# Performance work log

Measured on AMD Instinct MI355X. Metric: run time of the kernel, lower is better.

## Reference

```python
import jax, jax.numpy as jnp
import numpy as np

B = 65536
IN2 = 256      # input_shape * 2
H2 = 512       # rnn_hidden_dim * 2
A = 32         # n_actions


def setup_inputs() -> dict:
    key = jax.random.key(0)
    ks = jax.random.split(key, 12)
    s = lambda k, shape, fan: jax.random.normal(k, shape, jnp.float32) / np.sqrt(fan)
    return {
        "inputs": jax.random.normal(ks[0], (B, IN2), jnp.float32),
        "hidden_state": jax.random.normal(ks[1], (B, H2), jnp.float32),
        "W1": s(ks[2], (H2, IN2), IN2),
        "b1": jnp.zeros((H2,), jnp.float32),
        "W_ih": s(ks[3], (3 * H2, H2), H2),
        "W_hh": s(ks[4], (3 * H2, H2), H2),
        "b_ih": jnp.zeros((3 * H2,), jnp.float32),
        "b_hh": jnp.zeros((3 * H2,), jnp.float32),
        "W21": s(ks[5], (A, H2), H2),
        "b21": jnp.zeros((A,), jnp.float32),
        "W22": s(ks[6], (A, H2), H2),
        "b22": jnp.zeros((A,), jnp.float32),
    }


def _forward(inputs, hidden_state, W1, b1, W_ih, W_hh, b_ih, b_hh, W21, b21, W22, b22):
    # fc1 + ReLU
    x = jax.nn.relu(inputs @ W1.T + b1)                      # [B, H2]
    h_in = hidden_state.reshape(-1, H2)
    # PyTorch GRUCell semantics
    gi = x @ W_ih.T + b_ih                                   # [B, 3*H2]
    gh = h_in @ W_hh.T + b_hh                                # [B, 3*H2]
    i_r, i_z, i_n = jnp.split(gi, 3, axis=1)
    h_r, h_z, h_n = jnp.split(gh, 3, axis=1)
    r = jax.nn.sigmoid(i_r + h_r)
    z = jax.nn.sigmoid(i_z + h_z)
    n = jnp.tanh(i_n + r * h_n)
    h = (1.0 - z) * n + z * h_in                             # [B, H2]
    # two Q heads
    q1 = h @ W21.T + b21                                     # [B, A]
    q2 = h @ W22.T + b22                                     # [B, A]
    # vectorized row-interleave (replaces the nested Python loop)
    q = jnp.stack([q1, q2], axis=1).reshape(2 * q1.shape[0], q1.shape[1])  # [2B, A]
    return q, h


def reference(inputs, hidden_state, W1, b1, W_ih, W_hh, b_ih, b_hh, W21, b21, W22, b22):
    return _forward(inputs, hidden_state, W1, b1, W_ih, W_hh, b_ih, b_hh, W21, b21, W22, b22)
```

## Files before the change

kernel.cpp:

```cpp
#include <hip/hip_runtime.h>


#define BATCH 65536
#define IN2   256
#define H2    512
#define NA    32
#define QELEMS (2 * BATCH * NA)

typedef float  f32x4  __attribute__((ext_vector_type(4)));
typedef short  short8 __attribute__((ext_vector_type(8)));
typedef __bf16 bf16x8 __attribute__((ext_vector_type(8)));

__device__ __forceinline__ f32x4 mfma16(short8 a, short8 b, f32x4 c) {
  return __builtin_amdgcn_mfma_f32_16x16x32_bf16(
      __builtin_bit_cast(bf16x8, a), __builtin_bit_cast(bf16x8, b), c, 0, 0, 0);
}

__device__ __forceinline__ unsigned short f2bf(float f) {
  union { float f; unsigned u; } v; v.f = f;
  unsigned r = v.u + 0x7fffu + ((v.u >> 16) & 1u);
  return (unsigned short)(r >> 16);
}
__device__ __forceinline__ float bf2f(unsigned short u) {
  union { unsigned u; float f; } v; v.u = ((unsigned)u) << 16; return v.f;
}

__device__ __forceinline__ void gload16(const void* g, void* l) {
  __builtin_amdgcn_global_load_lds(
      (const __attribute__((address_space(1))) void*)g,
      (__attribute__((address_space(3))) void*)l, 16, 0, 0);
}

__device__ __forceinline__ float sigm(float x) {
  return 1.f / (1.f + __expf(-x));
}
__device__ __forceinline__ float tanh_fast(float x) {
  float t = __expf(-2.f * fabsf(x));
  float r = (1.f - t) / (1.f + t);
  return x >= 0.f ? r : -r;
}

__global__ void cvt_kernel(const float* __restrict__ s,
                           unsigned short* __restrict__ d, int n4) {
  for (int i = blockIdx.x * blockDim.x + threadIdx.x; i < n4;
       i += gridDim.x * blockDim.x) {
    float4 f = ((const float4*)s)[i];
    ushort4 o;
    o.x = f2bf(f.x); o.y = f2bf(f.y); o.z = f2bf(f.z); o.w = f2bf(f.w);
    ((ushort4*)d)[i] = o;
  }
}

__global__ void cvtw_kernel(const float* __restrict__ W1,
                            const float* __restrict__ Wih,
                            const float* __restrict__ Whh,
                            const float* __restrict__ W21,
                            const float* __restrict__ W22,
                            unsigned short* __restrict__ dW1,
                            unsigned short* __restrict__ dWih,
                            unsigned short* __restrict__ dWhh,
                            unsigned short* __restrict__ dW21,
                            unsigned short* __restrict__ dW22) {
  int i = blockIdx.x * blockDim.x + threadIdx.x;
  const float* s; unsigned short* d; int local;
  if      (i < 32768)  { s = W1;  d = dW1;  local = i; }
  else if (i < 229376) { s = Wih; d = dWih; local = i - 32768; }
  else if (i < 425984) { s = Whh; d = dWhh; local = i - 229376; }
  else if (i < 430080) { s = W21; d = dW21; local = i - 425984; }
  else if (i < 434176) { s = W22; d = dW22; local = i - 430080; }
  else return;
  float4 f = ((const float4*)s)[local];
  ushort4 o;
  o.x = f2bf(f.x); o.y = f2bf(f.y); o.z = f2bf(f.z); o.w = f2bf(f.w);
  ((ushort4*)d)[local] = o;
}

__global__ __launch_bounds__(256, 2)
void fc1_kernel(const float* __restrict__ A,
                const unsigned short* __restrict__ W,
                const float* __restrict__ bias,
                unsigned short* __restrict__ X) {
  __shared__ unsigned short As[128][72];
  __shared__ unsigned short Bs[64][72];
  const int tid  = threadIdx.x;
  const int lane = tid & 63, wid = tid >> 6;
  const int l16 = lane & 15, kg = (lane >> 4) * 8, rbase = (lane >> 4) * 4;
  const int row0 = blockIdx.x * 128;
  const int col0 = blockIdx.y * 64;
  const int wrow = (wid >> 1) * 64;
  const int wcol = (wid & 1) * 32;

  f32x4 acc[4][2] = {};

  for (int k0 = 0; k0 < IN2; k0 += 64) {
#pragma unroll
    for (int c = 0; c < 4; ++c) {
      int idx = tid + c * 256;
      int r = idx >> 3, k8 = idx & 7;
      const float* src = &A[(size_t)(row0 + r) * IN2 + k0 + k8 * 8];
      float4 f0 = *(const float4*)src;
      float4 f1 = *(const float4*)(src + 4);
      uint4 o;
      o.x = f2bf(f0.x) | ((unsigned)f2bf(f0.y) << 16);
      o.y = f2bf(f0.z) | ((unsigned)f2bf(f0.w) << 16);
      o.z = f2bf(f1.x) | ((unsigned)f2bf(f1.y) << 16);
      o.w = f2bf(f1.z) | ((unsigned)f2bf(f1.w) << 16);
      *(uint4*)&As[r][k8 * 8] = o;
    }
#pragma unroll
    for (int c = 0; c < 2; ++c) {
      int idx = tid + c * 256;
      int r = idx >> 3, k8 = idx & 7;
      *(uint4*)&Bs[r][k8 * 8] =
          *(const uint4*)&W[(size_t)(col0 + r) * IN2 + k0 + k8 * 8];
    }
    __syncthreads();
#pragma unroll
    for (int kk = 0; kk < 64; kk += 32) {
      short8 af[4], bf[2];
#pragma unroll
      for (int m = 0; m < 4; ++m)
        af[m] = *(const short8*)&As[wrow + m * 16 + l16][kk + kg];
#pragma unroll
      for (int n = 0; n < 2; ++n)
        bf[n] = *(const short8*)&Bs[wcol + n * 16 + l16][kk + kg];
#pragma unroll
      for (int m = 0; m < 4; ++m)
#pragma unroll
        for (int n = 0; n < 2; ++n)
          acc[m][n] = mfma16(af[m], bf[n], acc[m][n]);
    }
    __syncthreads();
  }

#pragma unroll
  for (int m = 0; m < 4; ++m)
#pragma unroll
    for (int n = 0; n < 2; ++n) {
      int col = col0 + wcol + n * 16 + l16;
      float bv = bias[col];
#pragma unroll
      for (int e = 0; e < 4; ++e) {
        int row = row0 + wrow + m * 16 + rbase + e;
        float v = acc[m][n][e] + bv;
        v = v > 0.f ? v : 0.f;
        X[(size_t)row * H2 + col] = f2bf(v);
      }
    }
}

__global__ __launch_bounds__(256, 2)
void gru_kernel(const unsigned short* __restrict__ X16,
                const unsigned short* __restrict__ H16,
                const unsigned short* __restrict__ Wih,
                const unsigned short* __restrict__ Whh,
                const float* __restrict__ b_ih,
                const float* __restrict__ b_hh,
                float* __restrict__ out_h,
                unsigned short* __restrict__ h16b) {
  __shared__ unsigned short lds[40960];
  char* ldsb = (char*)lds;

  const int tid  = threadIdx.x;
  const int lane = tid & 63, wid = tid >> 6;
  const int l16 = lane & 15;
  const int row0 = blockIdx.x * 128;
  const int j0   = blockIdx.y * 64;
  const int wrow = (wid >> 1) * 64;
  const int wcol = (wid & 1) * 32;

  const int lr   = lane >> 3;
  const int scol = ((lane & 7) ^ (lr & 7)) * 8;
  const unsigned short* gx = X16 + (size_t)(row0 + wid * 32 + lr) * H2 + scol;
  const unsigned short* gh = H16 + (size_t)(row0 + wid * 32 + lr) * H2 + scol;

  f32x4 accR[4][2] = {}, accZ[4][2] = {}, accIN[4][2] = {}, accHN[4][2] = {};

  for (int k0 = 0; k0 < H2; k0 += 64) {
#pragma unroll
    for (int i = 0; i < 4; ++i) {
      gload16(gx + k0 + i * 8 * H2, ldsb + (wid * 4 + i) * 1024);
      gload16(gh + k0 + i * 8 * H2, ldsb + 16384 + (wid * 4 + i) * 1024);
    }
#pragma unroll
    for (int i = 0; i < 12; ++i) {
      int g = wid * 12 + i;
      int s = g >> 3;
      int r = (g & 7) * 8 + lr;
      const unsigned short* src =
          (s < 3) ? Wih + (size_t)(s * H2 + j0 + r) * H2
                  : Whh + (size_t)((s - 3) * H2 + j0 + r) * H2;
      gload16(src + k0 + scol, ldsb + 32768 + g * 1024);
    }
    __syncthreads();

#pragma unroll
    for (int kk = 0; kk < 64; kk += 32) {
      const int cch = (kk >> 3) + (lane >> 4);
      short8 ax[4], ah[4];
#pragma unroll
      for (int m = 0; m < 4; ++m) {
        int r = wrow + m * 16 + l16;
        int off = r * 128 + ((cch ^ (r & 7)) << 4);
        ax[m] = *(const short8*)(ldsb + off);
        ah[m] = *(const short8*)(ldsb + 16384 + off);
      }
#pragma unroll
      for (int n = 0; n < 2; ++n) {
        int rr = wcol + n * 16 + l16;
        int woff = 32768 + rr * 128 + ((cch ^ (rr & 7)) << 4);
        short8 b0 = *(const short8*)(ldsb + woff);
        short8 b3 = *(const short8*)(ldsb + woff + 3 * 8192);
#pragma unroll
        for (int m = 0; m < 4; ++m) {
          accR[m][n] = mfma16(ax[m], b0, accR[m][n]);
          accR[m][n] = mfma16(ah[m], b3, accR[m][n]);
        }
        short8 b1 = *(const short8*)(ldsb + woff + 1 * 8192);
        short8 b4 = *(const short8*)(ldsb + woff + 4 * 8192);
#pragma unroll
        for (int m = 0; m < 4; ++m) {
          accZ[m][n] = mfma16(ax[m], b1, accZ[m][n]);
          accZ[m][n] = mfma16(ah[m], b4, accZ[m][n]);
        }
        short8 b2 = *(const short8*)(ldsb + woff + 2 * 8192);
        short8 b5 = *(const short8*)(ldsb + woff + 5 * 8192);
#pragma unroll
        for (int m = 0; m < 4; ++m) {
          accIN[m][n] = mfma16(ax[m], b2, accIN[m][n]);
          accHN[m][n] = mfma16(ah[m], b5, accHN[m][n]);
        }
      }
    }
    __syncthreads();
  }

  const int rbase = (lane >> 4) * 4;
#pragma unroll
  for (int n = 0; n < 2; ++n) {
    int j = j0 + wcol + n * 16 + l16;
    float brr = b_ih[j] + b_hh[j];
    float bzz = b_ih[H2 + j] + b_hh[H2 + j];
    float bin = b_ih[2 * H2 + j];
    float bhn = b_hh[2 * H2 + j];
#pragma unroll
    for (int m = 0; m < 4; ++m) {
#pragma unroll
      for (int e = 0; e < 4; ++e) {
        int row = row0 + wrow + m * 16 + rbase + e;
        float r  = sigm(accR[m][n][e] + brr);
        float z  = sigm(accZ[m][n][e] + bzz);
        float nn = tanh_fast(accIN[m][n][e] + bin + r * (accHN[m][n][e] + bhn));
        float hp = bf2f(H16[(size_t)row * H2 + j]);
        float h  = (1.f - z) * nn + z * hp;
        out_h[(size_t)row * H2 + j] = h;
        if (h16b) h16b[(size_t)row * H2 + j] = f2bf(h);
      }
    }
  }
}

__global__ __launch_bounds__(256, 2)
void heads_bf16_kernel(const unsigned short* __restrict__ Hsrc,
                       const unsigned short* __restrict__ Wq1,
                       const unsigned short* __restrict__ Wq2,
                       const float* __restrict__ b21,
                       const float* __restrict__ b22,
                       float* __restrict__ outq) {
  __shared__ unsigned short Hs[64][72];
  __shared__ unsigned short Wq[2][32][72];
  const int tid  = threadIdx.x;
  const int lane = tid & 63, wid = tid >> 6;
  const int l16 = lane & 15, kg = (lane >> 4) * 8, rbase = (lane >> 4) * 4;
  const int row0 = blockIdx.x * 64;
  const int wrow = wid * 16;

  f32x4 acc[2][2] = {};

  for (int k0 = 0; k0 < H2; k0 += 64) {
#pragma unroll
    for (int c = 0; c < 2; ++c) {
      int idx = tid + c * 256;
      int r = idx >> 3, k8 = idx & 7;
      *(uint4*)&Hs[r][k8 * 8] =
          *(const uint4*)&Hsrc[(size_t)(row0 + r) * H2 + k0 + k8 * 8];
    }
#pragma unroll
    for (int c = 0; c < 2; ++c) {
      int idx = tid + c * 256;
      int slab = idx >> 8, rem = idx & 255;
      int r = rem >> 3, k8 = rem & 7;
      const unsigned short* src = slab ? Wq2 : Wq1;
      *(uint4*)&Wq[slab][r][k8 * 8] =
          *(const uint4*)&src[(size_t)r * H2 + k0 + k8 * 8];
    }
    __syncthreads();
#pragma unroll
    for (int kk = 0; kk < 64; kk += 32) {
      short8 a = *(const short8*)&Hs[wrow + l16][kk + kg];
#pragma unroll
      for (int hd = 0; hd < 2; ++hd)
#pragma unroll
        for (int n = 0; n < 2; ++n) {
          short8 b = *(const short8*)&Wq[hd][n * 16 + l16][kk + kg];
          acc[hd][n] = mfma16(a, b, acc[hd][n]);
        }
    }
    __syncthreads();
  }

#pragma unroll
  for (int hd = 0; hd < 2; ++hd)
#pragma unroll
    for (int n = 0; n < 2; ++n) {
      int col = n * 16 + l16;
      float bv = hd ? b22[col] : b21[col];
#pragma unroll
      for (int e = 0; e < 4; ++e) {
        int row = row0 + wrow + rbase + e;
        outq[(size_t)(2 * row + hd) * NA + col] = acc[hd][n][e] + bv;
      }
    }
}

__global__ __launch_bounds__(256, 2)
void heads_f32_kernel(const float* __restrict__ Hsrc,
                      const unsigned short* __restrict__ Wq1,
                      const unsigned short* __restrict__ Wq2,
                      const float* __restrict__ b21,
                      const float* __restrict__ b22,
                      float* __restrict__ outq) {
  __shared__ unsigned short Hs[64][72];
  __shared__ unsigned short Wq[2][32][72];
  const int tid  = threadIdx.x;
  const int lane = tid & 63, wid = tid >> 6;
  const int l16 = lane & 15, kg = (lane >> 4) * 8, rbase = (lane >> 4) * 4;
  const int row0 = blockIdx.x * 64;
  const int wrow = wid * 16;

  f32x4 acc[2][2] = {};

  for (int k0 = 0; k0 < H2; k0 += 64) {
#pragma unroll
    for (int c = 0; c < 4; ++c) {
      int idx = tid + c * 256;
      int r = idx >> 4, c4 = idx & 15;
      float4 f = *(const float4*)&Hsrc[(size_t)(row0 + r) * H2 + k0 + c4 * 4];
      ushort4 o;
      o.x = f2bf(f.x); o.y = f2bf(f.y); o.z = f2bf(f.z); o.w = f2bf(f.w);
      *(ushort4*)&Hs[r][c4 * 4] = o;
    }
#pragma unroll
    for (int c = 0; c < 2; ++c) {
      int idx = tid + c * 256;
      int slab = idx >> 8, rem = idx & 255;
      int r = rem >> 3, k8 = rem & 7;
      const unsigned short* src = slab ? Wq2 : Wq1;
      *(uint4*)&Wq[slab][r][k8 * 8] =
          *(const uint4*)&src[(size_t)r * H2 + k0 + k8 * 8];
    }
    __syncthreads();
#pragma unroll
    for (int kk = 0; kk < 64; kk += 32) {
      short8 a = *(const short8*)&Hs[wrow + l16][kk + kg];
#pragma unroll
      for (int hd = 0; hd < 2; ++hd)
#pragma unroll
        for (int n = 0; n < 2; ++n) {
          short8 b = *(const short8*)&Wq[hd][n * 16 + l16][kk + kg];
          acc[hd][n] = mfma16(a, b, acc[hd][n]);
        }
    }
    __syncthreads();
  }

#pragma unroll
  for (int hd = 0; hd < 2; ++hd)
#pragma unroll
    for (int n = 0; n < 2; ++n) {
      int col = n * 16 + l16;
      float bv = hd ? b22[col] : b21[col];
#pragma unroll
      for (int e = 0; e < 4; ++e) {
        int row = row0 + wrow + rbase + e;
        outq[(size_t)(2 * row + hd) * NA + col] = acc[hd][n][e] + bv;
      }
    }
}

extern "C" void kernel_launch(void* const* d_in, const int* in_sizes, int n_in,
                              void* d_out, int out_size, void* d_ws,
                              size_t ws_size, hipStream_t stream) {
  (void)in_sizes; (void)n_in; (void)out_size;
  const float* inputs = (const float*)d_in[0];
  const float* hidden = (const float*)d_in[1];
  const float* W1     = (const float*)d_in[2];
  const float* b1     = (const float*)d_in[3];
  const float* W_ih   = (const float*)d_in[4];
  const float* W_hh   = (const float*)d_in[5];
  const float* b_ih   = (const float*)d_in[6];
  const float* b_hh   = (const float*)d_in[7];
  const float* W21    = (const float*)d_in[8];
  const float* b21    = (const float*)d_in[9];
  const float* W22    = (const float*)d_in[10];
  const float* b22    = (const float*)d_in[11];
  float* out = (float*)d_out;

  char* ws = (char*)d_ws;
  size_t off = 0;
  unsigned short* h16   = (unsigned short*)(ws + off); off += (size_t)BATCH * H2 * 2;
  unsigned short* x16   = (unsigned short*)(ws + off); off += (size_t)BATCH * H2 * 2;
  unsigned short* W1_16 = (unsigned short*)(ws + off); off += (size_t)H2 * IN2 * 2;
  unsigned short* Wih16 = (unsigned short*)(ws + off); off += (size_t)3 * H2 * H2 * 2;
  unsigned short* Whh16 = (unsigned short*)(ws + off); off += (size_t)3 * H2 * H2 * 2;
  unsigned short* W2116 = (unsigned short*)(ws + off); off += (size_t)NA * H2 * 2;
  unsigned short* W2216 = (unsigned short*)(ws + off); off += (size_t)NA * H2 * 2;
  size_t base_need = off;
  unsigned short* h16b = nullptr;
  if (ws_size >= base_need + (size_t)BATCH * H2 * 2)
    h16b = (unsigned short*)(ws + base_need);

  cvt_kernel<<<8192, 256, 0, stream>>>(hidden, h16, BATCH * H2 / 4);
  cvtw_kernel<<<1696, 256, 0, stream>>>(W1, W_ih, W_hh, W21, W22,
                                        W1_16, Wih16, Whh16, W2116, W2216);

  fc1_kernel<<<dim3(BATCH / 128, H2 / 64), 256, 0, stream>>>(inputs, W1_16, b1, x16);

  float* out_h = out + QELEMS;
  gru_kernel<<<dim3(BATCH / 128, H2 / 64), 256, 0, stream>>>(
      x16, h16, Wih16, Whh16, b_ih, b_hh, out_h, h16b);

  if (h16b)
    heads_bf16_kernel<<<BATCH / 64, 256, 0, stream>>>(h16b, W2116, W2216, b21, b22, out);
  else
    heads_f32_kernel<<<BATCH / 64, 256, 0, stream>>>(out_h, W2116, W2216, b21, b22, out);
}
```

Baseline: 644.2 us.

## Double-buffer fc1/GRU GEMMs, merge conversion kernels, restructure heads kernel

Merges the hidden-state and weight bf16 conversion kernels into one launch. Rewrites fc1 and the GRU GEMM with K=32 double-buffered LDS stages, an XOR swizzle, s_setprio around the MFMAs, and a block-index remap that groups column tiles for L2 reuse. The heads kernels now keep both Q-head weight matrices resident in LDS and read H fragments straight from global memory, with 128 rows per block. The aim is to overlap global loads with MFMA work and cut launch and sync overhead, at the cost of more LDS per block (80 KB for GRU) and possible occupancy limits.

```diff
diff --git a/kernel.cpp b/kernel.cpp
--- a/kernel.cpp
+++ b/kernel.cpp
@@ -10,6 +10,7 @@
 typedef float  f32x4  __attribute__((ext_vector_type(4)));
 typedef short  short8 __attribute__((ext_vector_type(8)));
 typedef __bf16 bf16x8 __attribute__((ext_vector_type(8)));
+typedef unsigned short ushort_t;
 
 __device__ __forceinline__ f32x4 mfma16(short8 a, short8 b, f32x4 c) {
   return __builtin_amdgcn_mfma_f32_16x16x32_bf16(
@@ -40,99 +41,117 @@
   return x >= 0.f ? r : -r;
 }
 
-__global__ void cvt_kernel(const float* __restrict__ s,
-                           unsigned short* __restrict__ d, int n4) {
-  for (int i = blockIdx.x * blockDim.x + threadIdx.x; i < n4;
+__global__ void cvt_all(const float* __restrict__ hid,
+                        const float* __restrict__ W1,
+                        const float* __restrict__ Wih,
+                        const float* __restrict__ Whh,
+                        const float* __restrict__ W21,
+                        const float* __restrict__ W22,
+                        ushort_t* __restrict__ h16,
+                        ushort_t* __restrict__ dW1,
+                        ushort_t* __restrict__ dWih,
+                        ushort_t* __restrict__ dWhh,
+                        ushort_t* __restrict__ dW21,
+                        ushort_t* __restrict__ dW22) {
+  for (int i = blockIdx.x * blockDim.x + threadIdx.x; i < 8822784;
        i += gridDim.x * blockDim.x) {
-    float4 f = ((const float4*)s)[i];
+    const float* s; ushort_t* d; int lo;
+    if (i < 8388608) { s = hid; d = h16; lo = i; }
+    else {
+      int k = i - 8388608;
+      if      (k < 32768)  { s = W1;  d = dW1;  lo = k; }
+      else if (k < 229376) { s = Wih; d = dWih; lo = k - 32768; }
+      else if (k < 425984) { s = Whh; d = dWhh; lo = k - 229376; }
+      else if (k < 430080) { s = W21; d = dW21; lo = k - 425984; }
+      else                 { s = W22; d = dW22; lo = k - 430080; }
+    }
+    float4 f = ((const float4*)s)[lo];
     ushort4 o;
     o.x = f2bf(f.x); o.y = f2bf(f.y); o.z = f2bf(f.z); o.w = f2bf(f.w);
-    ((ushort4*)d)[i] = o;
-  }
-}
-
-__global__ void cvtw_kernel(const float* __restrict__ W1,
-                            const float* __restrict__ Wih,
-                            const float* __restrict__ Whh,
-                            const float* __restrict__ W21,
-                            const float* __restrict__ W22,
-                            unsigned short* __restrict__ dW1,
-                            unsigned short* __restrict__ dWih,
-                            unsigned short* __restrict__ dWhh,
-                            unsigned short* __restrict__ dW21,
-                            unsigned short* __restrict__ dW22) {
-  int i = blockIdx.x * blockDim.x + threadIdx.x;
-  const float* s; unsigned short* d; int local;
-  if      (i < 32768)  { s = W1;  d = dW1;  local = i; }
-  else if (i < 229376) { s = Wih; d = dWih; local = i - 32768; }
-  else if (i < 425984) { s = Whh; d = dWhh; local = i - 229376; }
-  else if (i < 430080) { s = W21; d = dW21; local = i - 425984; }
-  else if (i < 434176) { s = W22; d = dW22; local = i - 430080; }
-  else return;
-  float4 f = ((const float4*)s)[local];
-  ushort4 o;
-  o.x = f2bf(f.x); o.y = f2bf(f.y); o.z = f2bf(f.z); o.w = f2bf(f.w);
-  ((ushort4*)d)[local] = o;
-}
-
-__global__ __launch_bounds__(256, 2)
+    ((ushort4*)d)[lo] = o;
+  }
+}
+
+__global__ __launch_bounds__(256, 4)
 void fc1_kernel(const float* __restrict__ A,
-                const unsigned short* __restrict__ W,
+                const ushort_t* __restrict__ W,
                 const float* __restrict__ bias,
-                unsigned short* __restrict__ X) {
-  __shared__ unsigned short As[128][72];
-  __shared__ unsigned short Bs[64][72];
+                ushort_t* __restrict__ X) {
+  __shared__ char ldsb[24576];
   const int tid  = threadIdx.x;
   const int lane = tid & 63, wid = tid >> 6;
-  const int l16 = lane & 15, kg = (lane >> 4) * 8, rbase = (lane >> 4) * 4;
-  const int row0 = blockIdx.x * 128;
-  const int col0 = blockIdx.y * 64;
+  const int l16  = lane & 15;
+  const int bid  = blockIdx.x;
+  const int lin  = (bid & 7) * 512 + (bid >> 3);
+  const int row0 = (lin >> 3) * 128;
+  const int col0 = (lin & 7) * 64;
   const int wrow = (wid >> 1) * 64;
   const int wcol = (wid & 1) * 32;
+  const int lr   = lane >> 2;
+  const int sc8  = ((lane & 3) ^ (lr & 3)) * 8;
+  const int rdx  = (((lane >> 4) ^ (lane & 3)) << 4);
 
   f32x4 acc[4][2] = {};
-
-  for (int k0 = 0; k0 < IN2; k0 += 64) {
-#pragma unroll
-    for (int c = 0; c < 4; ++c) {
-      int idx = tid + c * 256;
-      int r = idx >> 3, k8 = idx & 7;
-      const float* src = &A[(size_t)(row0 + r) * IN2 + k0 + k8 * 8];
-      float4 f0 = *(const float4*)src;
-      float4 f1 = *(const float4*)(src + 4);
+  float4 ra[2], rb[2];
+  char* buf0 = ldsb;
+  char* buf1 = ldsb + 12288;
+
+  auto LOADA = [&](int t) {
+#pragma unroll
+    for (int i = 0; i < 2; ++i) {
+      const float* p =
+          A + (size_t)(row0 + (wid * 2 + i) * 16 + lr) * IN2 + t * 32 + sc8;
+      ra[i] = *(const float4*)p;
+      rb[i] = *(const float4*)(p + 4);
+    }
+  };
+  auto GW = [&](int t, char* buf) {
+    const int jrow = col0 + wid * 16 + lr;
+    gload16(W + (size_t)jrow * IN2 + t * 32 + sc8, buf + 8192 + wid * 1024);
+  };
+  auto WRITEA = [&](char* buf) {
+#pragma unroll
+    for (int i = 0; i < 2; ++i) {
       uint4 o;
-      o.x = f2bf(f0.x) | ((unsigned)f2bf(f0.y) << 16);
-      o.y = f2bf(f0.z) | ((unsigned)f2bf(f0.w) << 16);
-      o.z = f2bf(f1.x) | ((unsigned)f2bf(f1.y) << 16);
-      o.w = f2bf(f1.z) | ((unsigned)f2bf(f1.w) << 16);
-      *(uint4*)&As[r][k8 * 8] = o;
-    }
-#pragma unroll
-    for (int c = 0; c < 2; ++c) {
-      int idx = tid + c * 256;
-      int r = idx >> 3, k8 = idx & 7;
-      *(uint4*)&Bs[r][k8 * 8] =
-          *(const uint4*)&W[(size_t)(col0 + r) * IN2 + k0 + k8 * 8];
-    }
+      o.x = f2bf(ra[i].x) | ((unsigned)f2bf(ra[i].y) << 16);
+      o.y = f2bf(ra[i].z) | ((unsigned)f2bf(ra[i].w) << 16);
+      o.z = f2bf(rb[i].x) | ((unsigned)f2bf(rb[i].y) << 16);
+      o.w = f2bf(rb[i].z) | ((unsigned)f2bf(rb[i].w) << 16);
+      *(uint4*)(buf + (wid * 2 + i) * 1024 + lane * 16) = o;
+    }
+  };
+  auto COMPUTE = [&](const char* buf) {
+    short8 af[4], bf[2];
+#pragma unroll
+    for (int m = 0; m < 4; ++m)
+      af[m] = *(const short8*)(buf + (wrow + m * 16 + l16) * 64 + rdx);
+#pragma unroll
+    for (int n = 0; n < 2; ++n)
+      bf[n] = *(const short8*)(buf + 8192 + (wcol + n * 16 + l16) * 64 + rdx);
+    __builtin_amdgcn_s_setprio(1);
+#pragma unroll
+    for (int m = 0; m < 4; ++m)
+#pragma unroll
+      for (int n = 0; n < 2; ++n)
+        acc[m][n] = mfma16(af[m], bf[n], acc[m][n]);
+    __builtin_amdgcn_s_setprio(0);
+  };
+
+  LOADA(0); GW(0, buf0); WRITEA(buf0);
+  __syncthreads();
+#pragma unroll 1
+  for (int t = 0; t < 8; t += 2) {
+    LOADA(t + 1); GW(t + 1, buf1);
+    COMPUTE(buf0);
+    WRITEA(buf1);
     __syncthreads();
-#pragma unroll
-    for (int kk = 0; kk < 64; kk += 32) {
-      short8 af[4], bf[2];
-#pragma unroll
-      for (int m = 0; m < 4; ++m)
-        af[m] = *(const short8*)&As[wrow + m * 16 + l16][kk + kg];
-#pragma unroll
-      for (int n = 0; n < 2; ++n)
-        bf[n] = *(const short8*)&Bs[wcol + n * 16 + l16][kk + kg];
-#pragma unroll
-      for (int m = 0; m < 4; ++m)
-#pragma unroll
-        for (int n = 0; n < 2; ++n)
-          acc[m][n] = mfma16(af[m], bf[n], acc[m][n]);
-    }
+    if (t + 2 < 8) { LOADA(t + 2); GW(t + 2, buf0); }
+    COMPUTE(buf1);
+    if (t + 2 < 8) WRITEA(buf0);
     __syncthreads();
   }
 
+  const int rbase = (lane >> 4) * 4;
 #pragma unroll
   for (int m = 0; m < 4; ++m)
 #pragma unroll
@@ -150,88 +169,98 @@
 }
 
 __global__ __launch_bounds__(256, 2)
-void gru_kernel(const unsigned short* __restrict__ X16,
-                const unsigned short* __restrict__ H16,
-                const unsigned short* __restrict__ Wih,
-                const unsigned short* __restrict__ Whh,
+void gru_kernel(const ushort_t* __restrict__ X16,
+                const ushort_t* __restrict__ H16,
+                const ushort_t* __restrict__ Wih,
+                const ushort_t* __restrict__ Whh,
                 const float* __restrict__ b_ih,
                 const float* __restrict__ b_hh,
                 float* __restrict__ out_h,
-                unsigned short* __restrict__ h16b) {
-  __shared__ unsigned short lds[40960];
-  char* ldsb = (char*)lds;
-
+                ushort_t* __restrict__ h16b) {
+  __shared__ char ldsb[81920];
   const int tid  = threadIdx.x;
   const int lane = tid & 63, wid = tid >> 6;
-  const int l16 = lane & 15;
-  const int row0 = blockIdx.x * 128;
-  const int j0   = blockIdx.y * 64;
+  const int l16  = lane & 15;
+  const int bid  = blockIdx.x;
+  const int lin  = (bid & 7) * 512 + (bid >> 3);
+  const int row0 = (lin >> 3) * 128;
+  const int j0   = (lin & 7) * 64;
   const int wrow = (wid >> 1) * 64;
   const int wcol = (wid & 1) * 32;
-
-  const int lr   = lane >> 3;
-  const int scol = ((lane & 7) ^ (lr & 7)) * 8;
-  const unsigned short* gx = X16 + (size_t)(row0 + wid * 32 + lr) * H2 + scol;
-  const unsigned short* gh = H16 + (size_t)(row0 + wid * 32 + lr) * H2 + scol;
+  const int lr   = lane >> 2;
+  const int sc8  = ((lane & 3) ^ (lr & 3)) * 8;
+  const int rdx  = (((lane >> 4) ^ (lane & 3)) << 4);
 
   f32x4 accR[4][2] = {}, accZ[4][2] = {}, accIN[4][2] = {}, accHN[4][2] = {};
 
-  for (int k0 = 0; k0 < H2; k0 += 64) {
-#pragma unroll
-    for (int i = 0; i < 4; ++i) {
-      gload16(gx + k0 + i * 8 * H2, ldsb + (wid * 4 + i) * 1024);
-      gload16(gh + k0 + i * 8 * H2, ldsb + 16384 + (wid * 4 + i) * 1024);
-    }
-#pragma unroll
-    for (int i = 0; i < 12; ++i) {
-      int g = wid * 12 + i;
-      int s = g >> 3;
-      int r = (g & 7) * 8 + lr;
-      const unsigned short* src =
-          (s < 3) ? Wih + (size_t)(s * H2 + j0 + r) * H2
-                  : Whh + (size_t)((s - 3) * H2 + j0 + r) * H2;
-      gload16(src + k0 + scol, ldsb + 32768 + g * 1024);
-    }
+  const int xc0 = wid * 2;
+  const size_t xrow0 = (size_t)(row0 + xc0 * 16 + lr) * H2 + sc8;
+
+  auto STAGE = [&](int t, char* buf) {
+    const int k0 = t * 32;
+#pragma unroll
+    for (int i = 0; i < 2; ++i) {
+      const int c = xc0 + i;
+      gload16(X16 + xrow0 + (size_t)i * 16 * H2 + k0, buf + c * 1024);
+      gload16(H16 + xrow0 + (size_t)i * 16 * H2 + k0, buf + 8192 + c * 1024);
+    }
+#pragma unroll
+    for (int i = 0; i < 6; ++i) {
+      const int g = wid * 6 + i;
+      const int p = g >> 2;
+      const int jrow = j0 + (g & 3) * 16 + lr;
+      const ushort_t* src = (p < 3)
+          ? Wih + (size_t)(p * H2 + jrow) * H2
+          : Whh + (size_t)((p - 3) * H2 + jrow) * H2;
+      gload16(src + k0 + sc8, buf + 16384 + g * 1024);
+    }
+  };
+
+  auto COMPUTE = [&](const char* buf) {
+    short8 ax[4], ah[4];
+#pragma unroll
+    for (int m = 0; m < 4; ++m) {
+      const int off = (wrow + m * 16 + l16) * 64 + rdx;
+      ax[m] = *(const short8*)(buf + off);
+      ah[m] = *(const short8*)(buf + 8192 + off);
+    }
+    __builtin_amdgcn_s_setprio(1);
+#pragma unroll
+    for (int n = 0; n < 2; ++n) {
+      const int woff = 16384 + (wcol + n * 16 + l16) * 64 + rdx;
+      short8 b0 = *(const short8*)(buf + woff);
+      short8 b1 = *(const short8*)(buf + woff + 4096);
+      short8 b2 = *(const short8*)(buf + woff + 8192);
+      short8 b3 = *(const short8*)(buf + woff + 12288);
+      short8 b4 = *(const short8*)(buf + woff + 16384);
+      short8 b5 = *(const short8*)(buf + woff + 20480);
+#pragma unroll
+      for (int m = 0; m < 4; ++m) accR[m][n] = mfma16(ax[m], b0, accR[m][n]);
+#pragma unroll
+      for (int m = 0; m < 4; ++m) accZ[m][n] = mfma16(ax[m], b1, accZ[m][n]);
+#pragma unroll
+      for (int m = 0; m < 4; ++m) accIN[m][n] = mfma16(ax[m], b2, accIN[m][n]);
+#pragma unroll
+      for (int m = 0; m < 4; ++m) accHN[m][n] = mfma16(ah[m], b5, accHN[m][n]);
+#pragma unroll
+      for (int m = 0; m < 4; ++m) accR[m][n] = mfma16(ah[m], b3, accR[m][n]);
+#pragma unroll
+      for (int m = 0; m < 4; ++m) accZ[m][n] = mfma16(ah[m], b4, accZ[m][n]);
+    }
+    __builtin_amdgcn_s_setprio(0);
+  };
+
+  char* buf0 = ldsb;
+  char* buf1 = ldsb + 40960;
+  STAGE(0, buf0);
+  __syncthreads();
+#pragma unroll 1
+  for (int t = 0; t < 16; t += 2) {
+    STAGE(t + 1, buf1);
+    COMPUTE(buf0);
     __syncthreads();
-
-#pragma unroll
-    for (int kk = 0; kk < 64; kk += 32) {
-      const int cch = (kk >> 3) + (lane >> 4);
-      short8 ax[4], ah[4];
-#pragma unroll
-      for (int m = 0; m < 4; ++m) {
-        int r = wrow + m * 16 + l16;
-        int off = r * 128 + ((cch ^ (r & 7)) << 4);
-        ax[m] = *(const short8*)(ldsb + off);
-        ah[m] = *(const short8*)(ldsb + 16384 + off);
-      }
-#pragma unroll
-      for (int n = 0; n < 2; ++n) {
-        int rr = wcol + n * 16 + l16;
-        int woff = 32768 + rr * 128 + ((cch ^ (rr & 7)) << 4);
-        short8 b0 = *(const short8*)(ldsb + woff);
-        short8 b3 = *(const short8*)(ldsb + woff + 3 * 8192);
-#pragma unroll
-        for (int m = 0; m < 4; ++m) {
-          accR[m][n] = mfma16(ax[m], b0, accR[m][n]);
-          accR[m][n] = mfma16(ah[m], b3, accR[m][n]);
-        }
-        short8 b1 = *(const short8*)(ldsb + woff + 1 * 8192);
-        short8 b4 = *(const short8*)(ldsb + woff + 4 * 8192);
-#pragma unroll
-        for (int m = 0; m < 4; ++m) {
-          accZ[m][n] = mfma16(ax[m], b1, accZ[m][n]);
-          accZ[m][n] = mfma16(ah[m], b4, accZ[m][n]);
-        }
-        short8 b2 = *(const short8*)(ldsb + woff + 2 * 8192);
-        short8 b5 = *(const short8*)(ldsb + woff + 5 * 8192);
-#pragma unroll
-        for (int m = 0; m < 4; ++m) {
-          accIN[m][n] = mfma16(ax[m], b2, accIN[m][n]);
-          accHN[m][n] = mfma16(ah[m], b5, accHN[m][n]);
-        }
-      }
-    }
+    if (t + 2 < 16) STAGE(t + 2, buf0);
+    COMPUTE(buf1);
     __syncthreads();
   }
 
@@ -261,131 +290,141 @@
 }
 
 __global__ __launch_bounds__(256, 2)
-void heads_bf16_kernel(const unsigned short* __restrict__ Hsrc,
-                       const unsigned short* __restrict__ Wq1,
-                       const unsigned short* __restrict__ Wq2,
+void heads_bf16_kernel(const ushort_t* __restrict__ Hsrc,
+                       const ushort_t* __restrict__ Wq1,
+                       const ushort_t* __restrict__ Wq2,
                        const float* __restrict__ b21,
                        const float* __restrict__ b22,
                        float* __restrict__ outq) {
-  __shared__ unsigned short Hs[64][72];
-  __shared__ unsigned short Wq[2][32][72];
+  __shared__ char WL[65536];
   const int tid  = threadIdx.x;
   const int lane = tid & 63, wid = tid >> 6;
-  const int l16 = lane & 15, kg = (lane >> 4) * 8, rbase = (lane >> 4) * 4;
-  const int row0 = blockIdx.x * 64;
-  const int wrow = wid * 16;
-
-  f32x4 acc[2][2] = {};
-
-  for (int k0 = 0; k0 < H2; k0 += 64) {
-#pragma unroll
-    for (int c = 0; c < 2; ++c) {
-      int idx = tid + c * 256;
-      int r = idx >> 3, k8 = idx & 7;
-      *(uint4*)&Hs[r][k8 * 8] =
-          *(const uint4*)&Hsrc[(size_t)(row0 + r) * H2 + k0 + k8 * 8];
-    }
-#pragma unroll
-    for (int c = 0; c < 2; ++c) {
-      int idx = tid + c * 256;
-      int slab = idx >> 8, rem = idx & 255;
-      int r = rem >> 3, k8 = rem & 7;
-      const unsigned short* src = slab ? Wq2 : Wq1;
-      *(uint4*)&Wq[slab][r][k8 * 8] =
-          *(const uint4*)&src[(size_t)r * H2 + k0 + k8 * 8];
-    }
-    __syncthreads();
-#pragma unroll
-    for (int kk = 0; kk < 64; kk += 32) {
-      short8 a = *(const short8*)&Hs[wrow + l16][kk + kg];
-#pragma unroll
-      for (int hd = 0; hd < 2; ++hd)
-#pragma unroll
-        for (int n = 0; n < 2; ++n) {
-          short8 b = *(const short8*)&Wq[hd][n * 16 + l16][kk + kg];
-          acc[hd][n] = mfma16(a, b, acc[hd][n]);
-        }
-    }
-    __syncthreads();
-  }
-
-#pragma unroll
-  for (int hd = 0; hd < 2; ++hd)
-#pragma unroll
-    for (int n = 0; n < 2; ++n) {
-      int col = n * 16 + l16;
-      float bv = hd ? b22[col] : b21[col];
+  const int l16  = lane & 15;
+  const int row0 = blockIdx.x * 128;
+  const int wrow = wid * 32;
+  const int kq   = lane >> 4;
+
+#pragma unroll
+  for (int i = 0; i < 16; ++i) {
+    const int g = wid * 16 + i;
+    const ushort_t* src =
+        (g < 32) ? Wq1 + (size_t)g * H2 : Wq2 + (size_t)(g - 32) * H2;
+    gload16(src + ((lane ^ (g & 7)) * 8), WL + g * 1024);
+  }
+  __syncthreads();
+
+  f32x4 acc[2][4] = {};
+#pragma unroll 2
+  for (int kc = 0; kc < 8; ++kc) {
+    short8 a[2][2];
+#pragma unroll
+    for (int m = 0; m < 2; ++m) {
+      const ushort_t* p =
+          Hsrc + (size_t)(row0 + wrow + m * 16 + l16) * H2 + kc * 64 + kq * 8;
+      a[0][m] = *(const short8*)p;
+      a[1][m] = *(const short8*)(p + 32);
+    }
+#pragma unroll
+    for (int kk = 0; kk < 2; ++kk) {
+      const int ckb = kc * 8 + kk * 4 + kq;
+#pragma unroll
+      for (int n = 0; n < 4; ++n) {
+        const int rr = n * 16 + l16;
+        short8 b = *(const short8*)(WL + rr * 1024 + ((ckb ^ (rr & 7)) << 4));
+#pragma unroll
+        for (int m = 0; m < 2; ++m)
+          acc[m][n] = mfma16(a[kk][m], b, acc[m][n]);
+      }
+    }
+  }
+
+  const int rbase = (lane >> 4) * 4;
+#pragma unroll
+  for (int n = 0; n < 4; ++n) {
+    const int hd  = n >> 1;
+    const int col = (n & 1) * 16 + l16;
+    const float bv = hd ? b22[col] : b21[col];
+#pragma unroll
+    for (int m = 0; m < 2; ++m)
 #pragma unroll
       for (int e = 0; e < 4; ++e) {
-        int row = row0 + wrow + rbase + e;
-        outq[(size_t)(2 * row + hd) * NA + col] = acc[hd][n][e] + bv;
-      }
-    }
+        const int row = row0 + wrow + m * 16 + rbase + e;
+        outq[(size_t)(2 * row + hd) * NA + col] = acc[m][n][e] + bv;
+      }
+  }
 }
 
 __global__ __launch_bounds__(256, 2)
 void heads_f32_kernel(const float* __restrict__ Hsrc,
-                      const unsigned short* __restrict__ Wq1,
-                      const unsigned short* __restrict__ Wq2,
+                      const ushort_t* __restrict__ Wq1,
+                      const ushort_t* __restrict__ Wq2,
                       const float* __restrict__ b21,
                       const float* __restrict__ b22,
                       float* __restrict__ outq) {
-  __shared__ unsigned short Hs[64][72];
-  __shared__ unsigned short Wq[2][32][72];
+  __shared__ char WL[65536];
   const int tid  = threadIdx.x;
   const int lane = tid & 63, wid = tid >> 6;
-  const int l16 = lane & 15, kg = (lane >> 4) * 8, rbase = (lane >> 4) * 4;
-  const int row0 = blockIdx.x * 64;
-  const int wrow = wid * 16;
-
-  f32x4 acc[2][2] = {};
-
-  for (int k0 = 0; k0 < H2; k0 += 64) {
-#pragma unroll
-    for (int c = 0; c < 4; ++c) {
-      int idx = tid + c * 256;
-      int r = idx >> 4, c4 = idx & 15;
-      float4 f = *(const float4*)&Hsrc[(size_t)(row0 + r) * H2 + k0 + c4 * 4];
-      ushort4 o;
-      o.x = f2bf(f.x); o.y = f2bf(f.y); o.z = f2bf(f.z); o.w = f2bf(f.w);
-      *(ushort4*)&Hs[r][c4 * 4] = o;
-    }
-#pragma unroll
-    for (int c = 0; c < 2; ++c) {
-      int idx = tid + c * 256;
-      int slab = idx >> 8, rem = idx & 255;
-      int r = rem >> 3, k8 = rem & 7;
-      const unsigned short* src = slab ? Wq2 : Wq1;
-      *(uint4*)&Wq[slab][r][k8 * 8] =
-          *(const uint4*)&src[(size_t)r * H2 + k0 + k8 * 8];
-    }
-    __syncthreads();
-#pragma unroll
-    for (int kk = 0; kk < 64; kk += 32) {
-      short8 a = *(const short8*)&Hs[wrow + l16][kk + kg];
-#pragma unroll
-      for (int hd = 0; hd < 2; ++hd)
-#pragma unroll
-        for (int n = 0; n < 2; ++n) {
-          short8 b = *(const short8*)&Wq[hd][n * 16 + l16][kk + kg];
-          acc[hd][n] = mfma16(a, b, acc[hd][n]);
-        }
-    }
-    __syncthreads();
-  }
-
-#pragma unroll
-  for (int hd = 0; hd < 2; ++hd)
-#pragma unroll
-    for (int n = 0; n < 2; ++n) {
-      int col = n * 16 + l16;
-      float bv = hd ? b22[col] : b21[col];
+  const int l16  = lane & 15;
+  const int row0 = blockIdx.x * 128;
+  const int wrow = wid * 32;
+  const int kq   = lane >> 4;
+
+#pragma unroll
+  for (int i = 0; i < 16; ++i) {
+    const int g = wid * 16 + i;
+    const ushort_t* src =
+        (g < 32) ? Wq1 + (size_t)g * H2 : Wq2 + (size_t)(g - 32) * H2;
+    gload16(src + ((lane ^ (g & 7)) * 8), WL + g * 1024);
+  }
+  __syncthreads();
+
+  f32x4 acc[2][4] = {};
+#pragma unroll 2
+  for (int kc = 0; kc < 8; ++kc) {
+    short8 a[2][2];
+#pragma unroll
+    for (int m = 0; m < 2; ++m)
+#pragma unroll
+      for (int kk = 0; kk < 2; ++kk) {
+        const float* p = Hsrc +
+            (size_t)(row0 + wrow + m * 16 + l16) * H2 + kc * 64 + kk * 32 + kq * 8;
+        float4 f0 = *(const float4*)p;
+        float4 f1 = *(const float4*)(p + 4);
+        uint4 o;
+        o.x = f2bf(f0.x) | ((unsigned)f2bf(f0.y) << 16);
+        o.y = f2bf(f0.z) | ((unsigned)f2bf(f0.w) << 16);
+        o.z = f2bf(f1.x) | ((unsigned)f2bf(f1.y) << 16);
+        o.w = f2bf(f1.z) | ((unsigned)f2bf(f1.w) << 16);
+        a[kk][m] = __builtin_bit_cast(short8, o);
+      }
+#pragma unroll
+    for (int kk = 0; kk < 2; ++kk) {
+      const int ckb = kc * 8 + kk * 4 + kq;
+#pragma unroll
+      for (int n = 0; n < 4; ++n) {
+        const int rr = n * 16 + l16;
+        short8 b = *(const short8*)(WL + rr * 1024 + ((ckb ^ (rr & 7)) << 4));
+#pragma unroll
+        for (int m = 0; m < 2; ++m)
+          acc[m][n] = mfma16(a[kk][m], b, acc[m][n]);
+      }
+    }
+  }
+
+  const int rbase = (lane >> 4) * 4;
+#pragma unroll
+  for (int n = 0; n < 4; ++n) {
+    const int hd  = n >> 1;
+    const int col = (n & 1) * 16 + l16;
+    const float bv = hd ? b22[col] : b21[col];
+#pragma unroll
+    for (int m = 0; m < 2; ++m)
 #pragma unroll
       for (int e = 0; e < 4; ++e) {
-        int row = row0 + wrow + rbase + e;
-        outq[(size_t)(2 * row + hd) * NA + col] = acc[hd][n][e] + bv;
-      }
-    }
+        const int row = row0 + wrow + m * 16 + rbase + e;
+        outq[(size_t)(2 * row + hd) * NA + col] = acc[m][n][e] + bv;
+      }
+  }
 }
 
 extern "C" void kernel_launch(void* const* d_in, const int* in_sizes, int n_in,
@@ -408,30 +447,31 @@
 
   char* ws = (char*)d_ws;
   size_t off = 0;
-  unsigned short* h16   = (unsigned short*)(ws + off); off += (size_t)BATCH * H2 * 2;
-  unsigned short* x16   = (unsigned short*)(ws + off); off += (size_t)BATCH * H2 * 2;
-  unsigned short* W1_16 = (unsigned short*)(ws + off); off += (size_t)H2 * IN2 * 2;
-  unsigned short* Wih16 = (unsigned short*)(ws + off); off += (size_t)3 * H2 * H2 * 2;
-  unsigned short* Whh16 = (unsigned short*)(ws + off); off += (size_t)3 * H2 * H2 * 2;
-  unsigned short* W2116 = (unsigned short*)(ws + off); off += (size_t)NA * H2 * 2;
-  unsigned short* W2216 = (unsigned short*)(ws + off); off += (size_t)NA * H2 * 2;
+  ushort_t* h16   = (ushort_t*)(ws + off); off += (size_t)BATCH * H2 * 2;
+  ushort_t* x16   = (ushort_t*)(ws + off); off += (size_t)BATCH * H2 * 2;
+  ushort_t* W1_16 = (ushort_t*)(ws + off); off += (size_t)H2 * IN2 * 2;
+  ushort_t* Wih16 = (ushort_t*)(ws + off); off += (size_t)3 * H2 * H2 * 2;
+  ushort_t* Whh16 = (ushort_t*)(ws + off); off += (size_t)3 * H2 * H2 * 2;
+  ushort_t* W2116 = (ushort_t*)(ws + off); off += (size_t)NA * H2 * 2;
+  ushort_t* W2216 = (ushort_t*)(ws + off); off += (size_t)NA * H2 * 2;
   size_t base_need = off;
-  unsigned short* h16b = nullptr;
+  ushort_t* h16b = nullptr;
   if (ws_size >= base_need + (size_t)BATCH * H2 * 2)
-    h16b = (unsigned short*)(ws + base_need);
-
-  cvt_kernel<<<8192, 256, 0, stream>>>(hidden, h16, BATCH * H2 / 4);
-  cvtw_kernel<<<1696, 256, 0, stream>>>(W1, W_ih, W_hh, W21, W22,
-                                        W1_16, Wih16, Whh16, W2116, W2216);
-
-  fc1_kernel<<<dim3(BATCH / 128, H2 / 64), 256, 0, stream>>>(inputs, W1_16, b1, x16);
+    h16b = (ushort_t*)(ws + base_need);
+
+  cvt_all<<<8192, 256, 0, stream>>>(hidden, W1, W_ih, W_hh, W21, W22,
+                                    h16, W1_16, Wih16, Whh16, W2116, W2216);
+
+  fc1_kernel<<<4096, 256, 0, stream>>>(inputs, W1_16, b1, x16);
 
   float* out_h = out + QELEMS;
-  gru_kernel<<<dim3(BATCH / 128, H2 / 64), 256, 0, stream>>>(
+  gru_kernel<<<4096, 256, 0, stream>>>(
       x16, h16, Wih16, Whh16, b_ih, b_hh, out_h, h16b);
 
   if (h16b)
-    heads_bf16_kernel<<<BATCH / 64, 256, 0, stream>>>(h16b, W2116, W2216, b21, b22, out);
+    heads_bf16_kernel<<<BATCH / 128, 256, 0, stream>>>(h16b, W2116, W2216,
+                                                       b21, b22, out);
   else
-    heads_f32_kernel<<<BATCH / 64, 256, 0, stream>>>(out_h, W2116, W2216, b21, b22, out);
-}
+    heads_f32_kernel<<<BATCH / 128, 256, 0, stream>>>(out_h, W2116, W2216,
+                                                      b21, b22, out);
+}
```

Measured after the change: 709.2 us. 1.1x slower.
